# Kernel optimization log

Measured on AMD Instinct MI355X. Metric: run time of the kernel, lower is better.

The kernel has to match this reference:

```python
import jax, jax.numpy as jnp
import numpy as np

B_, L_, H_, N_ = 8, 1024, 1024, 64

def setup_inputs() -> dict:
    key = jax.random.key(0)
    k1, k2, k3, k4 = jax.random.split(key, 4)
    return {
        "samples": jax.random.normal(k1, (B_, L_, 3 * H_), dtype=jnp.float32),
        "label_one_hot": jax.random.uniform(k2, (B_, L_, N_), dtype=jnp.float32),
        "predict": jax.random.normal(k3, (B_, L_, N_), dtype=jnp.float32),
        "W": jax.random.normal(k4, (H_, 3 * H_), dtype=jnp.float32) * (1.0 / np.sqrt(3 * H_)),
        "b_proj": jnp.zeros((H_,), dtype=jnp.float32),
    }

def reference(samples, label_one_hot, predict, W, b_proj):
    # projection: Linear(3H -> H)
    s = jnp.einsum("blk,hk->blh", samples, W) + b_proj          # [b,L,H]
    # dense similarity graph with diagonal masked out, row-softmax
    graph = jnp.einsum("blh,bmh->blm", s, s)                     # [b,L,L]
    L = graph.shape[1]
    eye = jnp.eye(L, dtype=graph.dtype)
    A = jax.nn.softmax(graph - 1e5 * eye, axis=-1)               # [b,L,L]
    # centered masked labels
    sup = label_one_hot
    row_has = (jnp.sum(sup, axis=-1) > 0.5).astype(sup.dtype)    # [b,L]
    total = jnp.sum(row_has, axis=-1)[:, None]                   # [b,1]
    avg = (jnp.sum(sup, axis=-2) / total)[:, None, :]            # [b,1,N]
    B0 = (sup - avg) * row_has[..., None]                        # [b,L,N]
    # diagonal inverse-degree scaling (elementwise, no dense diag matmul)
    d = 1.0 / (jnp.sum(A, axis=-1) + 1e-10)                      # [b,L]
    P = d[:, :, None] * jnp.swapaxes(A, -1, -2)                  # [b,L,L]
    Db = d[:, :, None] * B0                                      # [b,L,N]
    # 6-step power-iteration scan with residual injection at t==3
    ut = jnp.zeros_like(B0)
    for t in range(1, 7):
        ut = jnp.einsum("blm,bmn->bln", P, ut) + Db
        if t == 3:
            ut = ut + predict  # dropout is identity in eval mode
    return ut

if __name__ == "__main__":
    out = reference(**setup_inputs())
    print(out.shape, out.dtype)
```

## Files before the change

kernel.cpp:

```cpp
#include <hip/hip_runtime.h>


typedef _Float16 f16_t;
typedef f16_t f16x4 __attribute__((ext_vector_type(4)));
typedef f16_t f16x8 __attribute__((ext_vector_type(8)));
typedef float floatx4 __attribute__((ext_vector_type(4)));

__device__ __forceinline__ void async_copy16(const void* g, void* l) {
  __builtin_amdgcn_global_load_lds(
      (const __attribute__((address_space(1))) void*)g,
      (__attribute__((address_space(3))) void*)l, 16, 0, 0);
}

__device__ __forceinline__ f16_t hi_of(float x) { return (f16_t)x; }
__device__ __forceinline__ f16_t lo_of(float x, f16_t h) {
  return (f16_t)(x - (float)h);
}

__global__ __launch_bounds__(256) void prep_kernel(
    const float* __restrict__ W, f16_t* __restrict__ Whi, f16_t* __restrict__ Wlo,
    const float* __restrict__ samples, f16_t* __restrict__ SampH)
{
  const int bx = blockIdx.x, tid = threadIdx.x;
  if (bx < 3072) {
    const int i = bx * 256 + tid;
    float4 v = ((const float4*)W)[i];
    v.x *= 32.f; v.y *= 32.f; v.z *= 32.f; v.w *= 32.f;
    f16x4 h, l;
    f16_t h0 = hi_of(v.x); h[0] = h0; l[0] = lo_of(v.x, h0);
    f16_t h1 = hi_of(v.y); h[1] = h1; l[1] = lo_of(v.y, h1);
    f16_t h2 = hi_of(v.z); h[2] = h2; l[2] = lo_of(v.z, h2);
    f16_t h3 = hi_of(v.w); h[3] = h3; l[3] = lo_of(v.w, h3);
    *(f16x4*)(Whi + (size_t)i * 4) = h;
    *(f16x4*)(Wlo + (size_t)i * 4) = l;
  } else {
    const int i = (bx - 3072) * 256 + tid;
    const float4 v = ((const float4*)samples)[i];
    f16x4 h;
    h[0] = (f16_t)v.x; h[1] = (f16_t)v.y; h[2] = (f16_t)v.z; h[3] = (f16_t)v.w;
    *(f16x4*)(SampH + (size_t)i * 4) = h;
  }
}

struct Frags {
  f16x8 a[8];
  f16x8 bh0, bh1, bl0, bl1;
};

#define DSR(dst_, addr_, OFFSTR_) \
  asm volatile("ds_read_b128 %0, %1 offset:" OFFSTR_ : "=v"(dst_) : "v"(addr_))

__device__ __forceinline__ void read_frags_asm(unsigned sa, unsigned sb,
                                               Frags& f) {
  DSR(f.bh0, sb, "0");
  DSR(f.bh1, sb, "1024");
  DSR(f.bl0, sb, "8192");
  DSR(f.bl1, sb, "9216");
  DSR(f.a[0], sa, "0");
  DSR(f.a[1], sa, "1024");
  DSR(f.a[2], sa, "2048");
  DSR(f.a[3], sa, "3072");
  DSR(f.a[4], sa, "4096");
  DSR(f.a[5], sa, "5120");
  DSR(f.a[6], sa, "6144");
  DSR(f.a[7], sa, "7168");
}

__device__ __forceinline__ void mfma_all(const Frags& f, floatx4 acc[8][2]) {
  __builtin_amdgcn_s_setprio(1);
#pragma unroll
  for (int i = 0; i < 8; ++i) {
    acc[i][0] = __builtin_amdgcn_mfma_f32_16x16x32_f16(f.a[i], f.bh0, acc[i][0], 0, 0, 0);
    acc[i][1] = __builtin_amdgcn_mfma_f32_16x16x32_f16(f.a[i], f.bh1, acc[i][1], 0, 0, 0);
  }
#pragma unroll
  for (int i = 0; i < 8; ++i) {
    acc[i][0] = __builtin_amdgcn_mfma_f32_16x16x32_f16(f.a[i], f.bl0, acc[i][0], 0, 0, 0);
    acc[i][1] = __builtin_amdgcn_mfma_f32_16x16x32_f16(f.a[i], f.bl1, acc[i][1], 0, 0, 0);
  }
  __builtin_amdgcn_s_setprio(0);
}

__global__ __launch_bounds__(512, 2) void gemm1_pipe(
    const f16_t* __restrict__ Ag,
    const f16_t* __restrict__ BhG, const f16_t* __restrict__ BlG,
    const float* __restrict__ bias,
    f16_t* __restrict__ Chi, f16_t* __restrict__ Clo,
    int N, int K, float cscale)
{
  __shared__ __align__(16) char smem[131072];

  const int tid = threadIdx.x;
  const int lane = tid & 63;
  const int wave = tid >> 6;
  const int wm = wave >> 2;
  const int wn = wave & 3;
  const int m0 = blockIdx.y * 256;
  const int n0 = blockIdx.x * 128;
  const int fr = lane & 15;
  const int lch = lane >> 4;

  const int gA0 = tid;
  const int gA1 = tid + 512;
  const int rA0 = gA0 >> 2, lcA0 = (gA0 & 3) ^ ((rA0 >> 1) & 3);
  const int rA1 = gA1 >> 2, lcA1 = (gA1 & 3) ^ ((rA1 >> 1) & 3);
  const int rB = tid >> 2, lcB = (tid & 3) ^ ((rB >> 1) & 3);
  const f16_t* aSrc0 = Ag + (size_t)(m0 + rA0) * K + lcA0 * 8;
  const f16_t* aSrc1 = Ag + (size_t)(m0 + rA1) * K + lcA1 * 8;
  const f16_t* bhSrc = BhG + (size_t)(n0 + rB) * K + lcB * 8;
  const f16_t* blSrc = BlG + (size_t)(n0 + rB) * K + lcB * 8;
  char* ldsA0 = smem + gA0 * 16;
  char* ldsA1 = smem + gA1 * 16;
  char* ldsBh = smem + 16384 + (size_t)tid * 16;
  char* ldsBl = smem + 24576 + (size_t)tid * 16;

  const int swz = (lch ^ ((fr >> 1) & 3)) * 16;
  const int aoff = (wm * 128 + fr) * 64 + swz;
  const int boff = (wn * 32 + fr) * 64 + swz;
  const unsigned ldsBase =
      (unsigned)(size_t)(__attribute__((address_space(3))) char*)smem;
  const unsigned aA0 = ldsBase + (unsigned)aoff;
  const unsigned aA1 = aA0 + 32768u;
  const unsigned aA2 = aA0 + 65536u;
  const unsigned aA3 = aA0 + 98304u;
  const unsigned bA0 = ldsBase + 16384u + (unsigned)boff;
  const unsigned bA1 = bA0 + 32768u;
  const unsigned bA2 = bA0 + 65536u;
  const unsigned bA3 = bA0 + 98304u;

  floatx4 acc[8][2] = {};
  const int NS = K >> 5;

#define STAGE(SS_, SLOT_)                                     \
  do {                                                        \
    int ss = (SS_); if (ss >= NS) ss -= NS;                   \
    const int k0 = ss * 32;                                   \
    async_copy16(aSrc0 + k0, ldsA0 + (SLOT_) * 32768);        \
    async_copy16(aSrc1 + k0, ldsA1 + (SLOT_) * 32768);        \
    async_copy16(bhSrc + k0, ldsBh + (SLOT_) * 32768);        \
    async_copy16(blSrc + k0, ldsBl + (SLOT_) * 32768);        \
  } while (0)

#define HALF(SPRE_, SLOTPRE_, ARD_, BRD_, FRD_, FMM_)            \
  do {                                                           \
    STAGE(SPRE_, SLOTPRE_);                                      \
    asm volatile("s_waitcnt vmcnt(8)" ::: "memory");             \
    __builtin_amdgcn_s_barrier();                                \
    read_frags_asm(ARD_, BRD_, FRD_);                            \
    __builtin_amdgcn_sched_barrier(0);                           \
    asm volatile("s_waitcnt lgkmcnt(12)" ::: "memory");          \
    __builtin_amdgcn_sched_barrier(0);                           \
    mfma_all(FMM_, acc);                                         \
  } while (0)

  Frags f0, f1;

  STAGE(0, 0); STAGE(1, 1); STAGE(2, 2);
  asm volatile("s_waitcnt vmcnt(8)" ::: "memory");
  __builtin_amdgcn_s_barrier();
  read_frags_asm(aA0, bA0, f0);
  __builtin_amdgcn_sched_barrier(0);

  for (int s = 0; s < NS; s += 4) {
    HALF(s + 3, 3, aA1, bA1, f1, f0);
    HALF(s + 4, 0, aA2, bA2, f0, f1);
    HALF(s + 5, 1, aA3, bA3, f1, f0);
    HALF(s + 6, 2, aA0, bA0, f0, f1);
  }
  asm volatile("s_waitcnt vmcnt(0)" ::: "memory");
#undef HALF
#undef STAGE

  const int mr = (lane >> 4) * 4;
#pragma unroll
  for (int j = 0; j < 2; ++j) {
    const int n = n0 + wn * 32 + j * 16 + fr;
    const float bj = bias[n];
#pragma unroll
    for (int i = 0; i < 8; ++i) {
#pragma unroll
      for (int r = 0; r < 4; ++r) {
        const int m = m0 + wm * 128 + i * 16 + mr + r;
        float v = acc[i][j][r] * cscale + bj;
        f16_t h = hi_of(v);
        Chi[(size_t)m * N + n] = h;
        Clo[(size_t)m * N + n] = lo_of(v, h);
      }
    }
  }
}

template <int CMODE>
__global__ __launch_bounds__(256) void gemm_mfma(
    const f16_t* __restrict__ AhiG,
    const f16_t* __restrict__ BhiG, const f16_t* __restrict__ BloG,
    const float* __restrict__ bias,
    float* __restrict__ Cf, f16_t* __restrict__ Chi, f16_t* __restrict__ Clo,
    int M, int N, int K, long long sA, long long sB, long long sC, float cscale)
{
  AhiG += (long long)blockIdx.z * sA;
  BhiG += (long long)blockIdx.z * sB;
  BloG += (long long)blockIdx.z * sB;
  if (CMODE == 1) Cf += (long long)blockIdx.z * sC;

  __shared__ __align__(16) char smem[49152];
  f16_t* AsHi = (f16_t*)smem;
  f16_t* BsHi = (f16_t*)(smem + 16384);
  f16_t* BsLo = (f16_t*)(smem + 32768);

  const int tid = threadIdx.x;
  const int lane = tid & 63;
  const int wave = tid >> 6;
  const int wm = wave >> 1, wn = wave & 1;

  int m0, n0;
  if (CMODE == 0) {
    m0 = blockIdx.y * 128;
    n0 = blockIdx.x * 128;
  } else {
    int idx = blockIdx.x, i = 0, accu = 0;
    while (accu + i + 1 <= idx) { accu += i + 1; ++i; }
    m0 = i * 128;
    n0 = (idx - accu) * 128;
  }

  const int fr = lane & 15;
  const int kg = (lane >> 4) * 8;
  const int aoff = (wm * 64 + fr) * 32 + kg;
  const int boff = (wn * 64 + fr) * 32 + kg;

  floatx4 acc[4][4] = {};

  for (int k0 = 0; k0 < K; k0 += 64) {
    __syncthreads();
#pragma unroll
    for (int it = 0; it < 4; ++it) {
      const int cb = it * 256 + wave * 64;
      const int c = cb + lane;
      const int kk = c >> 9;
      const int row = (c >> 2) & 127;
      const int kc = kk * 32 + (c & 3) * 8;
      const size_t ga = (size_t)(m0 + row) * K + k0 + kc;
      const size_t gb = (size_t)(n0 + row) * K + k0 + kc;
      async_copy16(AhiG + ga, (char*)AsHi + (size_t)cb * 16);
      async_copy16(BhiG + gb, (char*)BsHi + (size_t)cb * 16);
      async_copy16(BloG + gb, (char*)BsLo + (size_t)cb * 16);
    }
    __syncthreads();

#pragma unroll
    for (int kk = 0; kk < 2; ++kk) {
      f16x8 ah[4], bh[4], bl[4];
#pragma unroll
      for (int t = 0; t < 4; ++t) {
        ah[t] = *(const f16x8*)&AsHi[kk * 4096 + aoff + t * 512];
        bh[t] = *(const f16x8*)&BsHi[kk * 4096 + boff + t * 512];
        bl[t] = *(const f16x8*)&BsLo[kk * 4096 + boff + t * 512];
      }
#pragma unroll
      for (int i = 0; i < 4; ++i)
#pragma unroll
        for (int j = 0; j < 4; ++j) {
          acc[i][j] = __builtin_amdgcn_mfma_f32_16x16x32_f16(ah[i], bh[j], acc[i][j], 0, 0, 0);
          acc[i][j] = __builtin_amdgcn_mfma_f32_16x16x32_f16(ah[i], bl[j], acc[i][j], 0, 0, 0);
        }
    }
  }

  const int mr = (lane >> 4) * 4;
#pragma unroll
  for (int j = 0; j < 4; ++j) {
    const int n = n0 + wn * 64 + j * 16 + fr;
    const float bj = (CMODE == 0) ? bias[n] : 0.f;
#pragma unroll
    for (int i = 0; i < 4; ++i) {
#pragma unroll
      for (int r = 0; r < 4; ++r) {
        const int m = m0 + wm * 64 + i * 16 + mr + r;
        float v = acc[i][j][r];
        if (CMODE == 0) {
          v = v * cscale + bj;
          f16_t h = hi_of(v);
          Chi[(size_t)m * N + n] = h;
          Clo[(size_t)m * N + n] = lo_of(v, h);
        } else {
          if (m == n) v -= 1e5f;
          Cf[(size_t)m * N + n] = v;
        }
      }
    }
  }

  if (CMODE == 1 && m0 != n0) {
    float* T = (float*)smem;
#pragma unroll
    for (int mc = 0; mc < 4; ++mc) {
      __syncthreads();
      if (wm == (mc >> 1)) {
        const int ibase = (mc & 1) * 2;
#pragma unroll
        for (int di = 0; di < 2; ++di) {
#pragma unroll
          for (int j = 0; j < 4; ++j) {
            const int nl = wn * 64 + j * 16 + fr;
#pragma unroll
            for (int r = 0; r < 4; ++r) {
              const int mloc = di * 16 + mr + r;
              T[nl * 36 + mloc] = acc[ibase + di][j][r];
            }
          }
        }
      }
      __syncthreads();
      const int row = tid >> 1, half = tid & 1;
      const float* src = &T[row * 36 + half * 16];
      float* dst = Cf + (size_t)(n0 + row) * N + m0 + mc * 32 + half * 16;
#pragma unroll
      for (int q = 0; q < 16; ++q) dst[q] = src[q];
    }
  }
}

__global__ __launch_bounds__(256) void rowstats_kernel(
    const float* __restrict__ G, float* __restrict__ mx, float* __restrict__ inv)
{
  __shared__ float red[4];
  const int tid = threadIdx.x;
  const float* g = G + (size_t)blockIdx.x * 1024;
  const float4 v = ((const float4*)g)[tid];

  float m = fmaxf(fmaxf(v.x, v.y), fmaxf(v.z, v.w));
#pragma unroll
  for (int off = 32; off > 0; off >>= 1) m = fmaxf(m, __shfl_down(m, off));
  if ((tid & 63) == 0) red[tid >> 6] = m;
  __syncthreads();
  m = fmaxf(fmaxf(red[0], red[1]), fmaxf(red[2], red[3]));
  __syncthreads();

  float s = __expf(v.x - m) + __expf(v.y - m) + __expf(v.z - m) + __expf(v.w - m);
#pragma unroll
  for (int off = 32; off > 0; off >>= 1) s += __shfl_down(s, off);
  if ((tid & 63) == 0) red[tid >> 6] = s;
  __syncthreads();
  if (tid == 0) {
    mx[blockIdx.x] = m;
    inv[blockIdx.x] = 1.0f / (red[0] + red[1] + red[2] + red[3]);
  }
}

__global__ __launch_bounds__(256) void make_at_kernel(
    const float* __restrict__ G, const float* __restrict__ mx,
    const float* __restrict__ inv, f16_t* __restrict__ At)
{
  const int row = blockIdx.x;
  const int b = row >> 10;
  const int tid = threadIdx.x;
  const float4 g = ((const float4*)(G + (size_t)row * 1024))[tid];
  const float4 m = ((const float4*)(mx + b * 1024))[tid];
  const float4 iv = ((const float4*)(inv + b * 1024))[tid];
  f16x4 o;
  o[0] = (f16_t)(__expf(g.x - m.x) * iv.x);
  o[1] = (f16_t)(__expf(g.y - m.y) * iv.y);
  o[2] = (f16_t)(__expf(g.z - m.z) * iv.z);
  o[3] = (f16_t)(__expf(g.w - m.w) * iv.w);
  *(f16x4*)(At + (size_t)row * 1024 + tid * 4) = o;
}

__global__ __launch_bounds__(1024) void make_db_kernel(
    const float* __restrict__ sup, float* __restrict__ Db, f16_t* __restrict__ DbT)
{
  const int L = 1024, Nn = 64;
  const float* s = sup + (size_t)blockIdx.x * L * Nn;
  float* db = Db + (size_t)blockIdx.x * L * Nn;
  f16_t* dbt = DbT + (size_t)blockIdx.x * L * Nn;
  __shared__ float rowhas[1024];
  __shared__ float cpart[1024];
  __shared__ float tpart[16];
  __shared__ float avg[64];
  __shared__ float totalsh;
  const int tid = threadIdx.x;

  const float4* sr = (const float4*)(s + (size_t)tid * 64);
  float ss = 0.f;
#pragma unroll
  for (int i = 0; i < 16; ++i) { const float4 v = sr[i]; ss += (v.x + v.y) + (v.z + v.w); }
  const float rh = (ss > 0.5f) ? 1.f : 0.f;
  rowhas[tid] = rh;
  float t = rh;
#pragma unroll
  for (int off = 32; off > 0; off >>= 1) t += __shfl_down(t, off);
  if ((tid & 63) == 0) tpart[tid >> 6] = t;

  const int n = tid & 63, seg = tid >> 6;
  float cs = 0.f;
  for (int l = seg * 64; l < seg * 64 + 64; ++l) cs += s[(size_t)l * 64 + n];
  cpart[seg * 64 + n] = cs;
  __syncthreads();
  if (tid == 0) { float tt = 0.f; for (int i = 0; i < 16; ++i) tt += tpart[i]; totalsh = tt; }
  __syncthreads();
  if (tid < 64) {
    float a = 0.f;
    for (int i = 0; i < 16; ++i) a += cpart[i * 64 + tid];
    avg[tid] = a / totalsh;
  }
  __syncthreads();

  const float4* s4 = (const float4*)s;
  float4* d4 = (float4*)db;
  for (int i = tid; i < (L * Nn) / 4; i += 1024) {
    float4 v = s4[i];
    const int l = i >> 4;
    const int nb = (i & 15) * 4;
    const float rhl = rowhas[l];
    v.x = (v.x - avg[nb + 0]) * rhl;
    v.y = (v.y - avg[nb + 1]) * rhl;
    v.z = (v.z - avg[nb + 2]) * rhl;
    v.w = (v.w - avg[nb + 3]) * rhl;
    d4[i] = v;
  }
  for (int i = tid; i < L * Nn; i += 1024) {
    const int n2 = i >> 10, l2 = i & 1023;
    dbt[i] = (f16_t)((s[(size_t)l2 * 64 + n2] - avg[n2]) * rowhas[l2]);
  }
}

__global__ __launch_bounds__(256) void iter_part(
    const f16_t* __restrict__ At, const f16_t* __restrict__ UT,
    float* __restrict__ Part)
{
  const int L = 1024, Nn = 64;
  const int b = blockIdx.y, l0 = blockIdx.x * 64, ks = blockIdx.z;
  At += (size_t)b * L * L;
  UT += (size_t)b * Nn * L;
  Part += (((size_t)ks * 8 + b) * L) * Nn;

  __shared__ __align__(16) f16_t AtS[2 * 64 * 32];
  __shared__ __align__(16) f16_t UtS[2 * 64 * 32];

  const int tid = threadIdx.x;
  const int lane = tid & 63;
  const int wave = tid >> 6;
  const int fr = lane & 15;
  const int kg = (lane >> 4) * 8;

  floatx4 acc[4] = {};

  for (int mi = 0; mi < 4; ++mi) {
    const int m0 = ks * 256 + mi * 64;
    __syncthreads();
#pragma unroll
    for (int it = 0; it < 2; ++it) {
      const int cb = it * 256 + wave * 64;
      const int c = cb + lane;
      const int kk = c >> 8;
      const int row = (c >> 2) & 63;
      const int kc = kk * 32 + (c & 3) * 8;
      async_copy16(At + (size_t)(l0 + row) * L + m0 + kc, (char*)AtS + (size_t)cb * 16);
      async_copy16(UT + (size_t)row * L + m0 + kc, (char*)UtS + (size_t)cb * 16);
    }
    __syncthreads();
#pragma unroll
    for (int kk = 0; kk < 2; ++kk) {
      const f16x8 a = *(const f16x8*)&AtS[kk * 2048 + (wave * 16 + fr) * 32 + kg];
#pragma unroll
      for (int j = 0; j < 4; ++j) {
        const f16x8 bf = *(const f16x8*)&UtS[kk * 2048 + (j * 16 + fr) * 32 + kg];
        acc[j] = __builtin_amdgcn_mfma_f32_16x16x32_f16(a, bf, acc[j], 0, 0, 0);
      }
    }
  }

  const int mr = (lane >> 4) * 4;
#pragma unroll
  for (int j = 0; j < 4; ++j) {
    const int n = j * 16 + fr;
#pragma unroll
    for (int r = 0; r < 4; ++r) {
      const int l = wave * 16 + mr + r;
      Part[(size_t)(l0 + l) * Nn + n] = acc[j][r];
    }
  }
}

template <int PRED, int FINAL>
__global__ __launch_bounds__(256) void iter_fin(
    const float* __restrict__ Part, const float* __restrict__ Db,
    const float* __restrict__ Pred, f16_t* __restrict__ UTn,
    float* __restrict__ OutF)
{
  const int L = 1024, Nn = 64;
  const int b = blockIdx.y, l0 = blockIdx.x * 64;
  const size_t base = ((size_t)b * L + l0) * Nn;
  const size_t ksStride = (size_t)8 * L * Nn;
  Db += base;
  if (PRED) Pred += base;

  __shared__ f16_t OutS[64 * 72];
  const int tid = threadIdx.x;

#pragma unroll
  for (int it = 0; it < 4; ++it) {
    const int idx = it * 256 + tid;
    const int l = idx >> 4, n4 = (idx & 15) * 4;
    const size_t o = (size_t)l * Nn + n4;
    float4 v = *(const float4*)(Part + base + o);
    const float4 p1 = *(const float4*)(Part + base + ksStride + o);
    const float4 p2 = *(const float4*)(Part + base + 2 * ksStride + o);
    const float4 p3 = *(const float4*)(Part + base + 3 * ksStride + o);
    v.x += p1.x; v.y += p1.y; v.z += p1.z; v.w += p1.w;
    v.x += p2.x; v.y += p2.y; v.z += p2.z; v.w += p2.w;
    v.x += p3.x; v.y += p3.y; v.z += p3.z; v.w += p3.w;
    const float4 d = *(const float4*)(Db + o);
    v.x += d.x; v.y += d.y; v.z += d.z; v.w += d.w;
    if (PRED) {
      const float4 p = *(const float4*)(Pred + o);
      v.x += p.x; v.y += p.y; v.z += p.z; v.w += p.w;
    }
    if (FINAL) {
      *(float4*)(OutF + base + o) = v;
    } else {
      OutS[(n4 + 0) * 72 + l] = (f16_t)v.x;
      OutS[(n4 + 1) * 72 + l] = (f16_t)v.y;
      OutS[(n4 + 2) * 72 + l] = (f16_t)v.z;
      OutS[(n4 + 3) * 72 + l] = (f16_t)v.w;
    }
  }
  if (!FINAL) {
    __syncthreads();
    f16_t* dst = UTn + (size_t)b * Nn * L;
#pragma unroll
    for (int it = 0; it < 2; ++it) {
      const int c = it * 256 + tid;
      const int n = c >> 3, lc = (c & 7) * 8;
      *(f16x8*)(dst + (size_t)n * L + l0 + lc) = *(const f16x8*)&OutS[n * 72 + lc];
    }
  }
}

extern "C" void kernel_launch(void* const* d_in, const int* in_sizes, int n_in,
                              void* d_out, int out_size, void* d_ws, size_t ws_size,
                              hipStream_t stream) {
  const float* samples = (const float*)d_in[0];
  const float* label   = (const float*)d_in[1];
  const float* predict = (const float*)d_in[2];
  const float* W       = (const float*)d_in[3];
  const float* bproj   = (const float*)d_in[4];
  float* out = (float*)d_out;

  char* ws = (char*)d_ws;
  f16_t* Whi = (f16_t*)ws;
  f16_t* Wlo = (f16_t*)(ws + 6291456);
  float* mx  = (float*)ws;
  float* inv = (float*)(ws + 32768);
  float* Db  = (float*)(ws + 65536);
  f16_t* DbT = (f16_t*)(ws + 65536 + 2097152);
  f16_t* UTa = (f16_t*)(ws + 65536 + 3145728);
  f16_t* UTb = (f16_t*)(ws + 65536 + 4194304);
  f16_t* SampH = (f16_t*)(ws + 12582912);
  float* G     = (float*)(ws + 12582912);
  f16_t* Shi = (f16_t*)(ws + 62914560);
  f16_t* Slo = (f16_t*)(ws + 62914560 + 16777216);
  f16_t* At  = Shi;
  float* Part = (float*)Slo;

  const long long LH = 1024LL * 1024;
  const long long LL = 1024LL * 1024;

  prep_kernel<<<dim3(27648), 256, 0, stream>>>(W, Whi, Wlo, samples, SampH);

  gemm1_pipe<<<dim3(8, 32), 512, 0, stream>>>(
      SampH, Whi, Wlo, bproj, Shi, Slo, 1024, 3072, 1.0f / 32.0f);

  gemm_mfma<1><<<dim3(36, 1, 8), 256, 0, stream>>>(
      Shi, Shi, Slo, nullptr, G, nullptr, nullptr,
      1024, 1024, 1024, LH, LH, LL, 1.0f);

  rowstats_kernel<<<8192, 256, 0, stream>>>(G, mx, inv);
  make_at_kernel<<<8192, 256, 0, stream>>>(G, mx, inv, At);

  make_db_kernel<<<8, 1024, 0, stream>>>(label, Db, DbT);

  dim3 gp(16, 8, 4), gf(16, 8);
  iter_part<<<gp, 256, 0, stream>>>(At, DbT, Part);
  iter_fin<0, 0><<<gf, 256, 0, stream>>>(Part, Db, nullptr, UTa, nullptr);
  iter_part<<<gp, 256, 0, stream>>>(At, UTa, Part);
  iter_fin<1, 0><<<gf, 256, 0, stream>>>(Part, Db, predict, UTb, nullptr);
  iter_part<<<gp, 256, 0, stream>>>(At, UTb, Part);
  iter_fin<0, 0><<<gf, 256, 0, stream>>>(Part, Db, nullptr, UTa, nullptr);
  iter_part<<<gp, 256, 0, stream>>>(At, UTa, Part);
  iter_fin<0, 0><<<gf, 256, 0, stream>>>(Part, Db, nullptr, UTb, nullptr);
  iter_part<<<gp, 256, 0, stream>>>(At, UTb, Part);
  iter_fin<0, 1><<<gf, 256, 0, stream>>>(Part, Db, nullptr, nullptr, out);
}
```

Before: 402.7 us.

## Restructure gemm1 main loop into split-phase granules with fewer fragment registers

Replaces the double-buffered register fragment scheme (two full Frags sets, reads overlapping the previous slice's MFMAs) with a single fragment set per k-slice. Each slice is split into two phases of 16 MFMAs, with LDS reads and global-to-LDS prefetches interleaved, separated by barriers and full lgkmcnt waits. This cuts VGPR pressure and spreads the global loads out. The cost is that LDS read latency is no longer hidden behind MFMAs, and there are more barriers per slice.

Result: no change. 401.3 us (-0.3%).

```diff
diff --git a/kernel.cpp b/kernel.cpp
--- a/kernel.cpp
+++ b/kernel.cpp
@@ -42,44 +42,8 @@
   }
 }
 
-struct Frags {
-  f16x8 a[8];
-  f16x8 bh0, bh1, bl0, bl1;
-};
-
 #define DSR(dst_, addr_, OFFSTR_) \
   asm volatile("ds_read_b128 %0, %1 offset:" OFFSTR_ : "=v"(dst_) : "v"(addr_))
-
-__device__ __forceinline__ void read_frags_asm(unsigned sa, unsigned sb,
-                                               Frags& f) {
-  DSR(f.bh0, sb, "0");
-  DSR(f.bh1, sb, "1024");
-  DSR(f.bl0, sb, "8192");
-  DSR(f.bl1, sb, "9216");
-  DSR(f.a[0], sa, "0");
-  DSR(f.a[1], sa, "1024");
-  DSR(f.a[2], sa, "2048");
-  DSR(f.a[3], sa, "3072");
-  DSR(f.a[4], sa, "4096");
-  DSR(f.a[5], sa, "5120");
-  DSR(f.a[6], sa, "6144");
-  DSR(f.a[7], sa, "7168");
-}
-
-__device__ __forceinline__ void mfma_all(const Frags& f, floatx4 acc[8][2]) {
-  __builtin_amdgcn_s_setprio(1);
-#pragma unroll
-  for (int i = 0; i < 8; ++i) {
-    acc[i][0] = __builtin_amdgcn_mfma_f32_16x16x32_f16(f.a[i], f.bh0, acc[i][0], 0, 0, 0);
-    acc[i][1] = __builtin_amdgcn_mfma_f32_16x16x32_f16(f.a[i], f.bh1, acc[i][1], 0, 0, 0);
-  }
-#pragma unroll
-  for (int i = 0; i < 8; ++i) {
-    acc[i][0] = __builtin_amdgcn_mfma_f32_16x16x32_f16(f.a[i], f.bl0, acc[i][0], 0, 0, 0);
-    acc[i][1] = __builtin_amdgcn_mfma_f32_16x16x32_f16(f.a[i], f.bl1, acc[i][1], 0, 0, 0);
-  }
-  __builtin_amdgcn_s_setprio(0);
-}
 
 __global__ __launch_bounds__(512, 2) void gemm1_pipe(
     const f16_t* __restrict__ Ag,
@@ -131,6 +95,9 @@
   floatx4 acc[8][2] = {};
   const int NS = K >> 5;
 
+  f16x8 bh0, bh1, bl0, bl1;
+  f16x8 a0_, a1_, a2_, a3_;
+
 #define STAGE(SS_, SLOT_)                                     \
   do {                                                        \
     int ss = (SS_); if (ss >= NS) ss -= NS;                   \
@@ -141,34 +108,86 @@
     async_copy16(blSrc + k0, ldsBl + (SLOT_) * 32768);        \
   } while (0)
 
-#define HALF(SPRE_, SLOTPRE_, ARD_, BRD_, FRD_, FMM_)            \
-  do {                                                           \
-    STAGE(SPRE_, SLOTPRE_);                                      \
-    asm volatile("s_waitcnt vmcnt(8)" ::: "memory");             \
-    __builtin_amdgcn_s_barrier();                                \
-    read_frags_asm(ARD_, BRD_, FRD_);                            \
-    __builtin_amdgcn_sched_barrier(0);                           \
-    asm volatile("s_waitcnt lgkmcnt(12)" ::: "memory");          \
-    __builtin_amdgcn_sched_barrier(0);                           \
-    mfma_all(FMM_, acc);                                         \
+#define SB0 __builtin_amdgcn_sched_barrier(0)
+
+#define MFMA16(MH_)                                                                               \
+  do {                                                                                            \
+    acc[4*(MH_)+0][0] = __builtin_amdgcn_mfma_f32_16x16x32_f16(a0_, bh0, acc[4*(MH_)+0][0],0,0,0);\
+    acc[4*(MH_)+0][1] = __builtin_amdgcn_mfma_f32_16x16x32_f16(a0_, bh1, acc[4*(MH_)+0][1],0,0,0);\
+    acc[4*(MH_)+1][0] = __builtin_amdgcn_mfma_f32_16x16x32_f16(a1_, bh0, acc[4*(MH_)+1][0],0,0,0);\
+    acc[4*(MH_)+1][1] = __builtin_amdgcn_mfma_f32_16x16x32_f16(a1_, bh1, acc[4*(MH_)+1][1],0,0,0);\
+    acc[4*(MH_)+2][0] = __builtin_amdgcn_mfma_f32_16x16x32_f16(a2_, bh0, acc[4*(MH_)+2][0],0,0,0);\
+    acc[4*(MH_)+2][1] = __builtin_amdgcn_mfma_f32_16x16x32_f16(a2_, bh1, acc[4*(MH_)+2][1],0,0,0);\
+    acc[4*(MH_)+3][0] = __builtin_amdgcn_mfma_f32_16x16x32_f16(a3_, bh0, acc[4*(MH_)+3][0],0,0,0);\
+    acc[4*(MH_)+3][1] = __builtin_amdgcn_mfma_f32_16x16x32_f16(a3_, bh1, acc[4*(MH_)+3][1],0,0,0);\
+    acc[4*(MH_)+0][0] = __builtin_amdgcn_mfma_f32_16x16x32_f16(a0_, bl0, acc[4*(MH_)+0][0],0,0,0);\
+    acc[4*(MH_)+0][1] = __builtin_amdgcn_mfma_f32_16x16x32_f16(a0_, bl1, acc[4*(MH_)+0][1],0,0,0);\
+    acc[4*(MH_)+1][0] = __builtin_amdgcn_mfma_f32_16x16x32_f16(a1_, bl0, acc[4*(MH_)+1][0],0,0,0);\
+    acc[4*(MH_)+1][1] = __builtin_amdgcn_mfma_f32_16x16x32_f16(a1_, bl1, acc[4*(MH_)+1][1],0,0,0);\
+    acc[4*(MH_)+2][0] = __builtin_amdgcn_mfma_f32_16x16x32_f16(a2_, bl0, acc[4*(MH_)+2][0],0,0,0);\
+    acc[4*(MH_)+2][1] = __builtin_amdgcn_mfma_f32_16x16x32_f16(a2_, bl1, acc[4*(MH_)+2][1],0,0,0);\
+    acc[4*(MH_)+3][0] = __builtin_amdgcn_mfma_f32_16x16x32_f16(a3_, bl0, acc[4*(MH_)+3][0],0,0,0);\
+    acc[4*(MH_)+3][1] = __builtin_amdgcn_mfma_f32_16x16x32_f16(a3_, bl1, acc[4*(MH_)+3][1],0,0,0);\
   } while (0)
 
-  Frags f0, f1;
+#define GRANULE(SPRE_, SLOTPRE_, AB_, BB_)                        \
+  do {                                                            \
+     \
+    DSR(bh0, BB_, "0");                                           \
+    DSR(bh1, BB_, "1024");                                        \
+    DSR(bl0, BB_, "8192");                                        \
+    DSR(bl1, BB_, "9216");                                        \
+    DSR(a0_, AB_, "0");                                           \
+    DSR(a1_, AB_, "1024");                                        \
+    DSR(a2_, AB_, "2048");                                        \
+    DSR(a3_, AB_, "3072");                                        \
+    {                                                             \
+      int ss = (SPRE_); if (ss >= NS) ss -= NS;                   \
+      const int k0 = ss * 32;                                     \
+      async_copy16(aSrc0 + k0, ldsA0 + (SLOTPRE_) * 32768);       \
+      async_copy16(aSrc1 + k0, ldsA1 + (SLOTPRE_) * 32768);       \
+    }                                                             \
+    __builtin_amdgcn_s_barrier();                                 \
+    asm volatile("s_waitcnt lgkmcnt(0)" ::: "memory");            \
+    SB0;                                                          \
+    __builtin_amdgcn_s_setprio(1);                                \
+    MFMA16(0);                                                    \
+    __builtin_amdgcn_s_setprio(0);                                \
+    __builtin_amdgcn_s_barrier();                                 \
+    \
+    DSR(a0_, AB_, "4096");                                        \
+    DSR(a1_, AB_, "5120");                                        \
+    DSR(a2_, AB_, "6144");                                        \
+    DSR(a3_, AB_, "7168");                                        \
+    {                                                             \
+      int ss = (SPRE_); if (ss >= NS) ss -= NS;                   \
+      const int k0 = ss * 32;                                     \
+      async_copy16(bhSrc + k0, ldsBh + (SLOTPRE_) * 32768);       \
+      async_copy16(blSrc + k0, ldsBl + (SLOTPRE_) * 32768);       \
+    }                                                             \
+    asm volatile("s_waitcnt vmcnt(8)" ::: "memory");              \
+    __builtin_amdgcn_s_barrier();                                 \
+    asm volatile("s_waitcnt lgkmcnt(0)" ::: "memory");            \
+    SB0;                                                          \
+    __builtin_amdgcn_s_setprio(1);                                \
+    MFMA16(1);                                                    \
+    __builtin_amdgcn_s_setprio(0);                                \
+    __builtin_amdgcn_s_barrier();                                 \
+  } while (0)
 
   STAGE(0, 0); STAGE(1, 1); STAGE(2, 2);
   asm volatile("s_waitcnt vmcnt(8)" ::: "memory");
   __builtin_amdgcn_s_barrier();
-  read_frags_asm(aA0, bA0, f0);
-  __builtin_amdgcn_sched_barrier(0);
 
   for (int s = 0; s < NS; s += 4) {
-    HALF(s + 3, 3, aA1, bA1, f1, f0);
-    HALF(s + 4, 0, aA2, bA2, f0, f1);
-    HALF(s + 5, 1, aA3, bA3, f1, f0);
-    HALF(s + 6, 2, aA0, bA0, f0, f1);
+    GRANULE(s + 3, 3, aA0, bA0);
+    GRANULE(s + 4, 0, aA1, bA1);
+    GRANULE(s + 5, 1, aA2, bA2);
+    GRANULE(s + 6, 2, aA3, bA3);
   }
   asm volatile("s_waitcnt vmcnt(0)" ::: "memory");
-#undef HALF
+#undef GRANULE
+#undef MFMA16
 #undef STAGE
 
   const int mr = (lane >> 4) * 4;
```
